# Performance work log

Hardware: AMD Instinct MI355X
Metric: run time of the kernel (lower is better)

## Reference

```python
import jax, jax.numpy as jnp
import numpy as np

C = 128            # in_channels
B, H, W = 4, 256, 256
WS = 8             # window_size
N = WS * WS        # tokens per window
HIDDEN = int(N ** 0.5) * 2   # WindowScoreBias hidden_dim = 16
NUM_HEADS = 2


def setup_inputs() -> dict:
    key = jax.random.key(0)
    ks = jax.random.split(key, 8)
    # deterministic relative-position table (mirrors _gen_window_score_bias_input, reduction=1)
    coords = np.stack(np.meshgrid(np.arange(WS), np.arange(WS), indexing='ij'), axis=2).reshape(N, 2)
    delta = (coords[:, None, :] - coords[None, :, :]).reshape(N * N, 2)
    uniq, index = np.unique(delta, axis=0, return_inverse=True)  # lexsorted unique == sorted tuples
    uniq = uniq.astype(np.float32) / np.abs(uniq).max()
    return {
        'x': jax.random.normal(ks[0], (B, C, H, W), jnp.float32),
        'delta': jnp.asarray(uniq),                       # [U, 2]
        'index': jnp.asarray(index.astype(np.int32)),     # [N*N]
        'w_qkv': jax.random.normal(ks[1], (3 * C, C), jnp.float32) * 0.02,
        'b_qkv': jnp.zeros((3 * C,), jnp.float32),
        'w_head': jax.random.normal(ks[2], (C, C), jnp.float32) * 0.02,
        'b_head': jnp.zeros((C,), jnp.float32),
        'w_b1': jax.random.normal(ks[3], (HIDDEN, 2), jnp.float32) * 0.02,
        'b_b1': jnp.zeros((HIDDEN,), jnp.float32),
        'w_b2': jax.random.normal(ks[4], (1, HIDDEN), jnp.float32) * 0.02,
        'b_b2': jnp.zeros((1,), jnp.float32),
        'w_c1': jax.random.normal(ks[5], (C, C, 1, 1), jnp.float32) * (2.0 / C) ** 0.5,
        'b_c1': jnp.zeros((C,), jnp.float32),
        'w_c2': jax.random.normal(ks[6], (C, C, 3, 3), jnp.float32) * (2.0 / (9 * C)) ** 0.5,
        'b_c2': jnp.zeros((C,), jnp.float32),
    }


def _conv(x, w, b):
    y = jax.lax.conv_general_dilated(x, w, (1, 1), 'VALID',
                                     dimension_numbers=('NCHW', 'OIHW', 'NCHW'))
    return y + b[None, :, None, None]


def reference(x, delta, index, w_qkv, b_qkv, w_head, b_head,
              w_b1, b_b1, w_b2, b_b2, w_c1, b_c1, w_c2, b_c2):
    Bx, Cx, Hx, Wx = x.shape
    oh, ow = Hx // WS, Wx // WS
    dk = Cx // NUM_HEADS
    # WindowScoreBias: MLP over unique deltas, gather by index -> [N, N]
    hmlp = jax.nn.gelu(delta @ w_b1.T + b_b1, approximate=False)
    bias = (hmlp @ w_b2.T + b_b2)[index].reshape(N, N)
    # window partition: BCHW -> (B*oh*ow, N, C)
    xw = x.reshape(Bx, Cx, oh, WS, ow, WS).transpose(0, 2, 4, 3, 5, 1).reshape(Bx * oh * ow, N, Cx)
    qkv = xw @ w_qkv.T + b_qkv
    q, k, v = jnp.split(qkv, 3, axis=-1)
    heads = lambda t: t.reshape(-1, N, NUM_HEADS, dk).transpose(0, 2, 1, 3)  # [Bw,h,N,dk]
    q, k, v = heads(q), heads(k), heads(v)
    scores = jnp.einsum('bhnd,bhmd->bhnm', q, k) * (1.0 / float(np.sqrt(dk))) + bias
    attn = jax.nn.softmax(scores, axis=-1)
    o = jnp.einsum('bhnm,bhmd->bhnd', attn, v)
    o = o.transpose(0, 2, 1, 3).reshape(-1, N, Cx) @ w_head.T + b_head
    # window reverse: (B*oh*ow, N, C) -> BCHW
    o = o.reshape(Bx, oh, ow, WS, WS, Cx).transpose(0, 5, 1, 3, 2, 4).reshape(Bx, Cx, Hx, Wx)
    x = x + o
    # conv_mlp: 1x1 conv -> GELU -> replication pad -> 3x3 conv -> LeakyReLU(0.1)
    y = jax.nn.gelu(_conv(x, w_c1, b_c1), approximate=False)
    y = jnp.pad(y, ((0, 0), (0, 0), (1, 1), (1, 1)), mode='edge')
    y = _conv(y, w_c2, b_c2)
    y = jnp.where(y > 0, y, 0.1 * y)
    return x + y
```

## Files before the change

### kernel.cpp

```cpp
#include <hip/hip_runtime.h>

typedef short v8s __attribute__((ext_vector_type(8)));
typedef float v4f __attribute__((ext_vector_type(4)));
typedef unsigned short v4u __attribute__((ext_vector_type(4)));

#define MFMA(a,b,c) __builtin_amdgcn_mfma_f32_16x16x32_bf16((a),(b),(c),0,0,0)

__device__ __forceinline__ unsigned short f2b(float f) {
  unsigned int x = __builtin_bit_cast(unsigned int, f);
  x += 0x7fffu + ((x >> 16) & 1u);
  return (unsigned short)(x >> 16);
}

__device__ __forceinline__ float b2f(unsigned short u) {
  unsigned int x = ((unsigned int)u) << 16;
  return __builtin_bit_cast(float, x);
}

__device__ __forceinline__ float gelu_exact(float v) {
  return 0.5f * v * (1.0f + erff(v * 0.70710678118654752f));
}

__global__ void prep_kernel(const float* __restrict__ wqkv, const float* __restrict__ whead,
                            const float* __restrict__ wc1, const float* __restrict__ wc2,
                            const float* __restrict__ delta, const int* __restrict__ indexv,
                            const float* __restrict__ wb1, const float* __restrict__ bb1,
                            const float* __restrict__ wb2, const float* __restrict__ bb2,
                            unsigned short* __restrict__ wqkv_b, unsigned short* __restrict__ whead_b,
                            unsigned short* __restrict__ wc1_b, unsigned short* __restrict__ w2r_b,
                            float* __restrict__ bias_ws) {
  int i = blockIdx.x * 256 + threadIdx.x;
  if (i < 49152) { wqkv_b[i] = f2b(wqkv[i]); return; }
  i -= 49152;
  if (i < 16384) { whead_b[i] = f2b(whead[i]); return; }
  i -= 16384;
  if (i < 16384) { wc1_b[i] = f2b(wc1[i]); return; }
  i -= 16384;
  if (i < 147456) {
    int o = i / 1152; int rem = i - o * 1152; int pos = rem >> 7; int c = rem & 127;
    w2r_b[i] = f2b(wc2[o * 1152 + c * 9 + pos]);
    return;
  }
  i -= 147456;
  if (i < 4096) {
    int u = indexv[i];
    float d0 = delta[2 * u], d1 = delta[2 * u + 1];
    float acc = bb2[0];
    #pragma unroll
    for (int j = 0; j < 16; ++j) {
      float t = d0 * wb1[2 * j] + d1 * wb1[2 * j + 1] + bb1[j];
      acc += gelu_exact(t) * wb2[j];
    }
    bias_ws[i] = acc;
  }
}

__global__ __launch_bounds__(256, 2) void xt_kernel(
    const float* __restrict__ x, unsigned short* __restrict__ t16) {
  __shared__ unsigned short T[256 * 129];
  const int tid = threadIdx.x;
  const int bid = blockIdx.x;
  const int b = bid >> 8, h = bid & 255;
  const float* src = x + (size_t)b * 128 * 65536 + h * 256;

  #pragma unroll
  for (int it = 0; it < 32; ++it) {
    int u = it * 256 + tid;
    int c = u >> 6, w4 = u & 63;
    float4 v = *(const float4*)(src + (size_t)c * 65536 + w4 * 4);
    int base = (w4 * 4) * 129 + c;
    T[base]       = f2b(v.x);
    T[base + 129] = f2b(v.y);
    T[base + 258] = f2b(v.z);
    T[base + 387] = f2b(v.w);
  }
  __syncthreads();

  unsigned short* dst = t16 + (size_t)((b * 256 + h) * 256) * 128;
  #pragma unroll
  for (int it = 0; it < 16; ++it) {
    int idx = it * 256 + tid;
    int px = idx >> 4, c8 = idx & 15;
    const unsigned short* t = &T[px * 129 + c8 * 8];
    v8s o;
    #pragma unroll
    for (int j = 0; j < 8; ++j) o[j] = (short)t[j];
    *(v8s*)(dst + px * 128 + c8 * 8) = o;
  }
}

__global__ __launch_bounds__(256, 3) void attn_kernel(
    const float* __restrict__ bias,
    const unsigned short* __restrict__ wqkv_b, const unsigned short* __restrict__ whead_b,
    const unsigned short* __restrict__ wc1_b,
    const float* __restrict__ bqkv, const float* __restrict__ bhead, const float* __restrict__ bc1,
    unsigned short* __restrict__ t16, unsigned short* __restrict__ ybuf) {
  __shared__ unsigned short U0[128 * 72];
  __shared__ unsigned short QP[64 * 136];
  __shared__ unsigned short KO[64 * 136];
  unsigned short* const XS = U0;
  unsigned short* const VT = U0;

  const int tid = threadIdx.x;
  const int wv = tid >> 6, lane = tid & 63, quad = lane >> 4, l15 = lane & 15;
  const int bid0 = blockIdx.x;
  const int bid = ((bid0 & 7) << 9) | (bid0 >> 3);
  const int bb = bid >> 10, rem = bid & 1023;
  const int h0 = (rem >> 5) * 8, w0 = (rem & 31) * 8;

  #pragma unroll
  for (int it = 0; it < 4; ++it) {
    int idx = it * 256 + tid;
    int token = idx >> 4, c8 = idx & 15;
    int py = token >> 3, px = token & 7;
    *(v8s*)(&XS[token * 136 + c8 * 8]) =
        *(const v8s*)(t16 + (size_t)((bb * 256 + h0 + py) * 256 + w0 + px) * 128 + c8 * 8);
  }
  __syncthreads();

  v4u vpk[2][4];
  #pragma unroll
  for (int part = 0; part < 3; ++part) {
    v4f acc[2][4] = {};
    #pragma unroll
    for (int ks = 0; ks < 4; ++ks) {
      v8s afr[2];
      #pragma unroll
      for (int i = 0; i < 2; ++i)
        afr[i] = *(const v8s*)(wqkv_b + (size_t)(part * 128 + (2 * wv + i) * 16 + l15) * 128 + ks * 32 + quad * 8);
      v8s bfr[4];
      #pragma unroll
      for (int ct = 0; ct < 4; ++ct)
        bfr[ct] = *(const v8s*)(&XS[(ct * 16 + l15) * 136 + ks * 32 + quad * 8]);
      #pragma unroll
      for (int i = 0; i < 2; ++i)
        #pragma unroll
        for (int ct = 0; ct < 4; ++ct)
          acc[i][ct] = MFMA(afr[i], bfr[ct], acc[i][ct]);
    }
    #pragma unroll
    for (int i = 0; i < 2; ++i) {
      int ol0 = (2 * wv + i) * 16 + quad * 4;
      float4 bq = *(const float4*)(bqkv + part * 128 + ol0);
      float bqa[4] = {bq.x, bq.y, bq.z, bq.w};
      #pragma unroll
      for (int ct = 0; ct < 4; ++ct) {
        int token = ct * 16 + l15;
        v4u pk = {f2b(acc[i][ct][0] + bqa[0]), f2b(acc[i][ct][1] + bqa[1]),
                  f2b(acc[i][ct][2] + bqa[2]), f2b(acc[i][ct][3] + bqa[3])};
        if (part == 0)      *(v4u*)(&QP[token * 136 + ol0]) = pk;
        else if (part == 1) *(v4u*)(&KO[token * 136 + ol0]) = pk;
        else                vpk[i][ct] = pk;
      }
    }
  }
  __syncthreads();

  #pragma unroll
  for (int i = 0; i < 2; ++i) {
    int ol0 = (2 * wv + i) * 16 + quad * 4;
    #pragma unroll
    for (int ct = 0; ct < 4; ++ct) {
      int token = ct * 16 + l15;
      VT[(ol0 + 0) * 72 + token] = vpk[i][ct][0];
      VT[(ol0 + 1) * 72 + token] = vpk[i][ct][1];
      VT[(ol0 + 2) * 72 + token] = vpk[i][ct][2];
      VT[(ol0 + 3) * 72 + token] = vpk[i][ct][3];
    }
  }

  const int t0 = wv * 16;
  v4f sc[2][4] = {};
  #pragma unroll
  for (int h = 0; h < 2; ++h)
    #pragma unroll
    for (int ks = 0; ks < 2; ++ks) {
      v8s afr = *(const v8s*)(&QP[(t0 + l15) * 136 + h * 64 + ks * 32 + quad * 8]);
      #pragma unroll
      for (int ct = 0; ct < 4; ++ct) {
        v8s bfr = *(const v8s*)(&KO[(ct * 16 + l15) * 136 + h * 64 + ks * 32 + quad * 8]);
        sc[h][ct] = MFMA(afr, bfr, sc[h][ct]);
      }
    }
  float linv[2][4];
  const int rowbase = (t0 + quad * 4) * 64 + l15;
  #pragma unroll
  for (int h = 0; h < 2; ++h) {
    float sv[4][4];
    #pragma unroll
    for (int ct = 0; ct < 4; ++ct)
      #pragma unroll
      for (int r = 0; r < 4; ++r)
        sv[ct][r] = sc[h][ct][r] * 0.125f + bias[rowbase + r * 64 + ct * 16];
    #pragma unroll
    for (int r = 0; r < 4; ++r) {
      float m = fmaxf(fmaxf(sv[0][r], sv[1][r]), fmaxf(sv[2][r], sv[3][r]));
      m = fmaxf(m, __shfl_xor(m, 1, 16));
      m = fmaxf(m, __shfl_xor(m, 2, 16));
      m = fmaxf(m, __shfl_xor(m, 4, 16));
      m = fmaxf(m, __shfl_xor(m, 8, 16));
      float s = 0.f;
      #pragma unroll
      for (int ct = 0; ct < 4; ++ct) { float p = __expf(sv[ct][r] - m); sv[ct][r] = p; s += p; }
      s += __shfl_xor(s, 1, 16);
      s += __shfl_xor(s, 2, 16);
      s += __shfl_xor(s, 4, 16);
      s += __shfl_xor(s, 8, 16);
      linv[h][r] = 1.0f / s;
    }
    #pragma unroll
    for (int ct = 0; ct < 4; ++ct)
      #pragma unroll
      for (int r = 0; r < 4; ++r)
        QP[(t0 + quad * 4 + r) * 136 + h * 64 + ct * 16 + l15] = f2b(sv[ct][r]);
  }
  __syncthreads();

  v4f ov[2][4] = {};
  #pragma unroll
  for (int h = 0; h < 2; ++h)
    #pragma unroll
    for (int ks = 0; ks < 2; ++ks) {
      v8s afr = *(const v8s*)(&QP[(t0 + l15) * 136 + h * 64 + ks * 32 + quad * 8]);
      #pragma unroll
      for (int ct = 0; ct < 4; ++ct) {
        v8s bfr = *(const v8s*)(&VT[(h * 64 + ct * 16 + l15) * 72 + ks * 32 + quad * 8]);
        ov[h][ct] = MFMA(afr, bfr, ov[h][ct]);
      }
    }
  #pragma unroll
  for (int h = 0; h < 2; ++h)
    #pragma unroll
    for (int ct = 0; ct < 4; ++ct)
      #pragma unroll
      for (int r = 0; r < 4; ++r)
        KO[(t0 + quad * 4 + r) * 136 + h * 64 + ct * 16 + l15] = f2b(ov[h][ct][r] * linv[h][r]);
  __syncthreads();

  v4f pj[8] = {};
  #pragma unroll
  for (int ks = 0; ks < 4; ++ks) {
    v8s afr = *(const v8s*)(&KO[(t0 + l15) * 136 + ks * 32 + quad * 8]);
    #pragma unroll
    for (int ct = 0; ct < 8; ++ct) {
      v8s bfr = *(const v8s*)(whead_b + (size_t)(ct * 16 + l15) * 128 + ks * 32 + quad * 8);
      pj[ct] = MFMA(afr, bfr, pj[ct]);
    }
  }
  {
    int token0 = t0 + quad * 4;
    int py = token0 >> 3, px = token0 & 7;
    const unsigned short* xtw = t16 + (size_t)((bb * 256 + h0 + py) * 256 + w0 + px) * 128;
    #pragma unroll
    for (int ct = 0; ct < 8; ++ct) {
      int o = ct * 16 + l15;
      float bh = bhead[o];
      #pragma unroll
      for (int r = 0; r < 4; ++r) {
        float xa = b2f(xtw[(size_t)r * 128 + o]);
        XS[(token0 + r) * 136 + o] = f2b(xa + pj[ct][r] + bh);
      }
    }
  }
  __syncthreads();

  #pragma unroll
  for (int it = 0; it < 4; ++it) {
    int idx = it * 256 + tid;
    int token = idx >> 4, c8 = idx & 15;
    int py = token >> 3, px = token & 7;
    *(v8s*)(t16 + (size_t)((bb * 256 + h0 + py) * 256 + w0 + px) * 128 + c8 * 8) =
        *(const v8s*)(&XS[token * 136 + c8 * 8]);
  }

  v4f c1[2][4] = {};
  #pragma unroll
  for (int ks = 0; ks < 4; ++ks) {
    v8s afr[2];
    #pragma unroll
    for (int i = 0; i < 2; ++i)
      afr[i] = *(const v8s*)(wc1_b + (size_t)((2 * wv + i) * 16 + l15) * 128 + ks * 32 + quad * 8);
    v8s bfr[4];
    #pragma unroll
    for (int ct = 0; ct < 4; ++ct)
      bfr[ct] = *(const v8s*)(&XS[(ct * 16 + l15) * 136 + ks * 32 + quad * 8]);
    #pragma unroll
    for (int i = 0; i < 2; ++i)
      #pragma unroll
      for (int ct = 0; ct < 4; ++ct)
        c1[i][ct] = MFMA(afr[i], bfr[ct], c1[i][ct]);
  }
  #pragma unroll
  for (int i = 0; i < 2; ++i) {
    int o0 = (2 * wv + i) * 16 + quad * 4;
    float4 bc = *(const float4*)(bc1 + o0);
    float bca[4] = {bc.x, bc.y, bc.z, bc.w};
    #pragma unroll
    for (int ct = 0; ct < 4; ++ct) {
      int pix = ct * 16 + l15, ppy = pix >> 3, ppx = pix & 7;
      unsigned short g[4];
      #pragma unroll
      for (int r = 0; r < 4; ++r) g[r] = f2b(gelu_exact(c1[i][ct][r] + bca[r]));
      v4u pk = {g[0], g[1], g[2], g[3]};
      *(v4u*)(ybuf + (size_t)((bb * 256 + h0 + ppy) * 256 + w0 + ppx) * 128 + o0) = pk;
    }
  }
}

__global__ __launch_bounds__(256, 4) void conv2_kernel(
    const unsigned short* __restrict__ w2r, const unsigned short* __restrict__ ybuf,
    const unsigned short* __restrict__ t16, const float* __restrict__ bc2, float* __restrict__ xo) {
  __shared__ unsigned short HALO[136 * 136];
  const int tid = threadIdx.x;
  const int wv = tid >> 6, lane = tid & 63, quad = lane >> 4, l15 = lane & 15;
  const int bid0 = blockIdx.x;
  const int bid = ((bid0 & 7) << 9) | (bid0 >> 3);
  const int bb = bid >> 10, rem = bid & 1023;
  const int y0 = (rem >> 3) * 2, x0 = (rem & 7) * 32;

  v4u xpre[2][4];
  #pragma unroll
  for (int i = 0; i < 2; ++i) {
    int o0 = (2 * wv + i) * 16 + quad * 4;
    #pragma unroll
    for (int ct = 0; ct < 4; ++ct) {
      int pix = ct * 16 + l15, typ = pix >> 5, txp = pix & 31;
      xpre[i][ct] = *(const v4u*)(t16 + (size_t)((bb * 256 + y0 + typ) * 256 + x0 + txp) * 128 + o0);
    }
  }

  for (int it = 0; it < 9; ++it) {
    int idx = it * 256 + tid;
    if (idx < 2176) {
      int hp = idx >> 4, c8 = idx & 15;
      int iy = hp / 34, ix = hp - iy * 34;
      int hy = y0 - 1 + iy; hy = hy < 0 ? 0 : (hy > 255 ? 255 : hy);
      int hx = x0 - 1 + ix; hx = hx < 0 ? 0 : (hx > 255 ? 255 : hx);
      *(v8s*)(&HALO[hp * 136 + c8 * 8]) =
          *(const v8s*)(ybuf + (size_t)((bb * 256 + hy) * 256 + hx) * 128 + c8 * 8);
    }
  }
  __syncthreads();

  v4f acc[2][4] = {};
  int bct[4];
  #pragma unroll
  for (int ct = 0; ct < 4; ++ct) {
    int pix = ct * 16 + l15, typ = pix >> 5, txp = pix & 31;
    bct[ct] = (typ * 34 + txp) * 136 + quad * 8;
  }
  const unsigned short* wb0 = w2r + (size_t)((2 * wv + 0) * 16 + l15) * 1152 + quad * 8;
  const unsigned short* wb1 = w2r + (size_t)((2 * wv + 1) * 16 + l15) * 1152 + quad * 8;
  #pragma unroll
  for (int ks = 0; ks < 36; ++ks) {
    const int pos = ks >> 2, cb = ks & 3;
    const int ky = pos / 3, kx = pos - ky * 3;
    const int koff = (ky * 34 + kx) * 136 + cb * 32;
    v8s a0 = *(const v8s*)(wb0 + ks * 32);
    v8s a1 = *(const v8s*)(wb1 + ks * 32);
    #pragma unroll
    for (int ct = 0; ct < 4; ++ct) {
      v8s bfr = *(const v8s*)(&HALO[bct[ct] + koff]);
      acc[0][ct] = MFMA(a0, bfr, acc[0][ct]);
      acc[1][ct] = MFMA(a1, bfr, acc[1][ct]);
    }
  }

  #pragma unroll
  for (int i = 0; i < 2; ++i) {
    int o0 = (2 * wv + i) * 16 + quad * 4;
    float4 bc = *(const float4*)(bc2 + o0);
    float bca[4] = {bc.x, bc.y, bc.z, bc.w};
    #pragma unroll
    for (int ct = 0; ct < 4; ++ct) {
      int pix = ct * 16 + l15, typ = pix >> 5, txp = pix & 31;
      float* po = xo + (size_t)(bb * 128 + o0) * 65536 + (y0 + typ) * 256 + (x0 + txp);
      #pragma unroll
      for (int r = 0; r < 4; ++r) {
        float v = acc[i][ct][r] + bca[r];
        v = v > 0.f ? v : 0.1f * v;
        po[(size_t)r * 65536] = v + b2f(xpre[i][ct][r]);
      }
    }
  }
}

extern "C" void kernel_launch(void* const* d_in, const int* in_sizes, int n_in,
                              void* d_out, int out_size, void* d_ws, size_t ws_size,
                              hipStream_t stream) {
  (void)in_sizes; (void)n_in; (void)out_size; (void)ws_size;
  const float* x      = (const float*)d_in[0];
  const float* delta  = (const float*)d_in[1];
  const int*   indexv = (const int*)d_in[2];
  const float* w_qkv  = (const float*)d_in[3];
  const float* b_qkv  = (const float*)d_in[4];
  const float* w_head = (const float*)d_in[5];
  const float* b_head = (const float*)d_in[6];
  const float* w_b1   = (const float*)d_in[7];
  const float* b_b1   = (const float*)d_in[8];
  const float* w_b2   = (const float*)d_in[9];
  const float* b_b2   = (const float*)d_in[10];
  const float* w_c1   = (const float*)d_in[11];
  const float* b_c1   = (const float*)d_in[12];
  const float* w_c2   = (const float*)d_in[13];
  const float* b_c2   = (const float*)d_in[14];
  float* out = (float*)d_out;

  char* ws = (char*)d_ws;
  float*          bias_ws = (float*)(ws + 0);
  unsigned short* wqkv_b  = (unsigned short*)(ws + 16384);
  unsigned short* whead_b = (unsigned short*)(ws + 114688);
  unsigned short* wc1_b   = (unsigned short*)(ws + 147456);
  unsigned short* w2r_b   = (unsigned short*)(ws + 180224);
  unsigned short* ybuf    = (unsigned short*)(ws + 475136);
  unsigned short* t16     = (unsigned short*)(ws + 475136 + 67108864);

  prep_kernel<<<912, 256, 0, stream>>>(w_qkv, w_head, w_c1, w_c2, delta, indexv,
                                       w_b1, b_b1, w_b2, b_b2,
                                       wqkv_b, whead_b, wc1_b, w2r_b, bias_ws);
  xt_kernel<<<1024, 256, 0, stream>>>(x, t16);
  attn_kernel<<<4096, 256, 0, stream>>>(bias_ws, wqkv_b, whead_b, wc1_b,
                                        b_qkv, b_head, b_c1, t16, ybuf);
  conv2_kernel<<<4096, 256, 0, stream>>>(w2r_b, ybuf, t16, b_c2, out);
}
```

Measured before the change: 693.1 us.

## Fuse 1x1 conv and GELU into 3x3 conv kernel with halo recompute

The 1x1 conv plus GELU moves out of the attention kernel and into the 3x3 conv kernel. That kernel now loads a 4x34 halo of the attention output (t16) into LDS and recomputes the 1x1 conv and GELU for every halo pixel into a second LDS buffer, which the 3x3 conv then reads. This drops the 64 MB bf16 ybuf intermediate, so its global write and re-read go away. The cost is roughly twice the 1x1 conv MFMA and erf work because of halo overlap, plus a doubled LDS footprint that lowers the occupancy hint from 4 blocks to 2.

```diff
diff --git a/kernel.cpp b/kernel.cpp
--- a/kernel.cpp
+++ b/kernel.cpp
@@ -92,9 +92,8 @@
 __global__ __launch_bounds__(256, 3) void attn_kernel(
     const float* __restrict__ bias,
     const unsigned short* __restrict__ wqkv_b, const unsigned short* __restrict__ whead_b,
-    const unsigned short* __restrict__ wc1_b,
-    const float* __restrict__ bqkv, const float* __restrict__ bhead, const float* __restrict__ bc1,
-    unsigned short* __restrict__ t16, unsigned short* __restrict__ ybuf) {
+    const float* __restrict__ bqkv, const float* __restrict__ bhead,
+    unsigned short* __restrict__ t16) {
   __shared__ unsigned short U0[128 * 72];
   __shared__ unsigned short QP[64 * 136];
   __shared__ unsigned short KO[64 * 136];
@@ -272,45 +271,14 @@
     *(v8s*)(t16 + (size_t)((bb * 256 + h0 + py) * 256 + w0 + px) * 128 + c8 * 8) =
         *(const v8s*)(&XS[token * 136 + c8 * 8]);
   }
-
-  v4f c1[2][4] = {};
-  #pragma unroll
-  for (int ks = 0; ks < 4; ++ks) {
-    v8s afr[2];
-    #pragma unroll
-    for (int i = 0; i < 2; ++i)
-      afr[i] = *(const v8s*)(wc1_b + (size_t)((2 * wv + i) * 16 + l15) * 128 + ks * 32 + quad * 8);
-    v8s bfr[4];
-    #pragma unroll
-    for (int ct = 0; ct < 4; ++ct)
-      bfr[ct] = *(const v8s*)(&XS[(ct * 16 + l15) * 136 + ks * 32 + quad * 8]);
-    #pragma unroll
-    for (int i = 0; i < 2; ++i)
-      #pragma unroll
-      for (int ct = 0; ct < 4; ++ct)
-        c1[i][ct] = MFMA(afr[i], bfr[ct], c1[i][ct]);
-  }
-  #pragma unroll
-  for (int i = 0; i < 2; ++i) {
-    int o0 = (2 * wv + i) * 16 + quad * 4;
-    float4 bc = *(const float4*)(bc1 + o0);
-    float bca[4] = {bc.x, bc.y, bc.z, bc.w};
-    #pragma unroll
-    for (int ct = 0; ct < 4; ++ct) {
-      int pix = ct * 16 + l15, ppy = pix >> 3, ppx = pix & 7;
-      unsigned short g[4];
-      #pragma unroll
-      for (int r = 0; r < 4; ++r) g[r] = f2b(gelu_exact(c1[i][ct][r] + bca[r]));
-      v4u pk = {g[0], g[1], g[2], g[3]};
-      *(v4u*)(ybuf + (size_t)((bb * 256 + h0 + ppy) * 256 + w0 + ppx) * 128 + o0) = pk;
-    }
-  }
-}
-
-__global__ __launch_bounds__(256, 4) void conv2_kernel(
-    const unsigned short* __restrict__ w2r, const unsigned short* __restrict__ ybuf,
-    const unsigned short* __restrict__ t16, const float* __restrict__ bc2, float* __restrict__ xo) {
-  __shared__ unsigned short HALO[136 * 136];
+}
+
+__global__ __launch_bounds__(256, 2) void conv2_kernel(
+    const unsigned short* __restrict__ w2r, const unsigned short* __restrict__ wc1_b,
+    const unsigned short* __restrict__ t16,
+    const float* __restrict__ bc1, const float* __restrict__ bc2, float* __restrict__ xo) {
+  __shared__ unsigned short XH[144 * 136];
+  __shared__ unsigned short YH[144 * 136];
   const int tid = threadIdx.x;
   const int wv = tid >> 6, lane = tid & 63, quad = lane >> 4, l15 = lane & 15;
   const int bid0 = blockIdx.x;
@@ -336,8 +304,42 @@
       int iy = hp / 34, ix = hp - iy * 34;
       int hy = y0 - 1 + iy; hy = hy < 0 ? 0 : (hy > 255 ? 255 : hy);
       int hx = x0 - 1 + ix; hx = hx < 0 ? 0 : (hx > 255 ? 255 : hx);
-      *(v8s*)(&HALO[hp * 136 + c8 * 8]) =
-          *(const v8s*)(ybuf + (size_t)((bb * 256 + hy) * 256 + hx) * 128 + c8 * 8);
+      *(v8s*)(&XH[hp * 136 + c8 * 8]) =
+          *(const v8s*)(t16 + (size_t)((bb * 256 + hy) * 256 + hx) * 128 + c8 * 8);
+    }
+  }
+  __syncthreads();
+
+  v4f yacc[2][9] = {};
+  #pragma unroll
+  for (int ks = 0; ks < 4; ++ks) {
+    v8s afr[2];
+    #pragma unroll
+    for (int i = 0; i < 2; ++i)
+      afr[i] = *(const v8s*)(wc1_b + (size_t)((2 * wv + i) * 16 + l15) * 128 + ks * 32 + quad * 8);
+    v8s bfr[9];
+    #pragma unroll
+    for (int ct = 0; ct < 9; ++ct)
+      bfr[ct] = *(const v8s*)(&XH[(ct * 16 + l15) * 136 + ks * 32 + quad * 8]);
+    #pragma unroll
+    for (int i = 0; i < 2; ++i)
+      #pragma unroll
+      for (int ct = 0; ct < 9; ++ct)
+        yacc[i][ct] = MFMA(afr[i], bfr[ct], yacc[i][ct]);
+  }
+  #pragma unroll
+  for (int i = 0; i < 2; ++i) {
+    int ol0 = (2 * wv + i) * 16 + quad * 4;
+    float4 bq = *(const float4*)(bc1 + ol0);
+    float bqa[4] = {bq.x, bq.y, bq.z, bq.w};
+    #pragma unroll
+    for (int ct = 0; ct < 9; ++ct) {
+      int token = ct * 16 + l15;
+      v4u pk = {f2b(gelu_exact(yacc[i][ct][0] + bqa[0])),
+                f2b(gelu_exact(yacc[i][ct][1] + bqa[1])),
+                f2b(gelu_exact(yacc[i][ct][2] + bqa[2])),
+                f2b(gelu_exact(yacc[i][ct][3] + bqa[3]))};
+      *(v4u*)(&YH[token * 136 + ol0]) = pk;
     }
   }
   __syncthreads();
@@ -360,7 +362,7 @@
     v8s a1 = *(const v8s*)(wb1 + ks * 32);
     #pragma unroll
     for (int ct = 0; ct < 4; ++ct) {
-      v8s bfr = *(const v8s*)(&HALO[bct[ct] + koff]);
+      v8s bfr = *(const v8s*)(&YH[bct[ct] + koff]);
       acc[0][ct] = MFMA(a0, bfr, acc[0][ct]);
       acc[1][ct] = MFMA(a1, bfr, acc[1][ct]);
     }
@@ -412,14 +414,13 @@
   unsigned short* whead_b = (unsigned short*)(ws + 114688);
   unsigned short* wc1_b   = (unsigned short*)(ws + 147456);
   unsigned short* w2r_b   = (unsigned short*)(ws + 180224);
-  unsigned short* ybuf    = (unsigned short*)(ws + 475136);
   unsigned short* t16     = (unsigned short*)(ws + 475136 + 67108864);
 
   prep_kernel<<<912, 256, 0, stream>>>(w_qkv, w_head, w_c1, w_c2, delta, indexv,
                                        w_b1, b_b1, w_b2, b_b2,
                                        wqkv_b, whead_b, wc1_b, w2r_b, bias_ws);
   xt_kernel<<<1024, 256, 0, stream>>>(x, t16);
-  attn_kernel<<<4096, 256, 0, stream>>>(bias_ws, wqkv_b, whead_b, wc1_b,
-                                        b_qkv, b_head, b_c1, t16, ybuf);
-  conv2_kernel<<<4096, 256, 0, stream>>>(w2r_b, ybuf, t16, b_c2, out);
-}
+  attn_kernel<<<4096, 256, 0, stream>>>(bias_ws, wqkv_b, whead_b,
+                                        b_qkv, b_head, t16);
+  conv2_kernel<<<4096, 256, 0, stream>>>(w2r_b, wc1_b, t16, b_c1, b_c2, out);
+}
```

New measurement: 619.8 us. -10.6%, faster.
